# Optimization experiments

Hardware: AMD Instinct MI355X
Metric: run time of the kernel (lower is better)

Reference implementation:

```python
import jax, jax.numpy as jnp
import numpy as np

BLOCK_SIZE = 32
FP6_E2M3_MAX = 7.5

def _build_fp6_e2m3_grid():
    vals = set()
    for bits in range(64):
        s = (bits >> 5) & 1
        e = (bits >> 3) & 3
        m = bits & 7
        v = (m / 8.0) if e == 0 else (1.0 + m / 8.0) * 2.0 ** (e - 1)
        vals.add(-v if s else v)
    return np.array(sorted(vals), dtype=np.float32)

_GRID = jnp.asarray(_build_fp6_e2m3_grid())  # sorted 1-D fp32 grid (46 unique values)

def _nearest_on_grid(x, grid):
    # round-to-nearest on a sorted grid via searchsorted (matches torch reference)
    idx = jnp.clip(jnp.searchsorted(grid, x), 0, grid.shape[0] - 1)
    idx_lo = jnp.maximum(idx - 1, 0)
    v_hi = grid[idx]
    v_lo = grid[idx_lo]
    return jnp.where(jnp.abs(x - v_lo) <= jnp.abs(x - v_hi), v_lo, v_hi)

def _mx_quantize(t, eps=1e-30):
    # t: (rows, K) fp32, K divisible by BLOCK_SIZE
    rows, K = t.shape
    blocks = t.reshape(rows, K // BLOCK_SIZE, BLOCK_SIZE)
    scales = jnp.maximum(jnp.max(jnp.abs(blocks), axis=-1) / FP6_E2M3_MAX, eps)  # (rows, nb)
    q = _nearest_on_grid(blocks / scales[..., None], _GRID)  # fp6-simulated fp32
    return q, scales

def setup_inputs() -> dict:
    key = jax.random.key(0)
    k1, k2, k3 = jax.random.split(key, 3)
    x = jax.random.normal(k1, (8, 8192, 1024), dtype=jnp.float32)
    weight = jax.random.normal(k2, (1024, 1024), dtype=jnp.float32) * 0.02
    bias = jax.random.normal(k3, (1024,), dtype=jnp.float32) * 0.02
    return {"x": x, "weight": weight, "bias": bias}

def reference(x, weight, bias):
    batch_shape = x.shape[:-1]
    in_features = x.shape[-1]
    x2 = x.astype(jnp.float32).reshape(-1, in_features)      # (N, K)
    w2 = weight.astype(jnp.float32)                           # (J, K)
    xq, xs = _mx_quantize(x2)                                 # (N, nb, bs), (N, nb)
    wq, ws = _mx_quantize(w2)                                 # (J, nb, bs), (J, nb)
    # out[n, j] = sum_b xs[n,b] * ws[j,b] * dot(xq[n,b,:], wq[j,b,:])
    # == dequant(x) @ dequant(w).T  (fold fp32 scales into quantized blocks)
    xd = (xq * xs[..., None]).reshape(x2.shape)
    wd = (wq * ws[..., None]).reshape(w2.shape)
    out = xd @ wd.T + bias
    return out.reshape(*batch_shape, -1)
```

## Files before the change

kernel.cpp:

```cpp
#include <hip/hip_runtime.h>
#include <stdint.h>

#define K_DIM 1024
#define N_DIM 1024
#define M_DIM 65536

typedef __bf16 bf16_t;
typedef __bf16 bf16x8 __attribute__((ext_vector_type(8)));
typedef float f32x4 __attribute__((ext_vector_type(4)));

#define GLOAD_LDS16(g, l) __builtin_amdgcn_global_load_lds( \
    (const __attribute__((address_space(1))) void*)(g),     \
    (__attribute__((address_space(3))) void*)(l), 16, 0, 0)

__global__ __launch_bounds__(256) void quant_dequant_kernel(
    const float* __restrict__ in, bf16_t* __restrict__ out, long long nvec) {
  long long i = (long long)blockIdx.x * blockDim.x + threadIdx.x;
  long long stride = (long long)gridDim.x * blockDim.x;
  for (; i < nvec; i += stride) {
    long long base = i * 8;
    f32x4 v0 = *reinterpret_cast<const f32x4*>(in + base);
    f32x4 v1 = *reinterpret_cast<const f32x4*>(in + base + 4);
    float mx = 0.0f;
#pragma unroll
    for (int j = 0; j < 4; ++j) {
      mx = fmaxf(mx, fabsf(v0[j]));
      mx = fmaxf(mx, fabsf(v1[j]));
    }
    mx = fmaxf(mx, __shfl_xor(mx, 1));
    mx = fmaxf(mx, __shfl_xor(mx, 2));
    float s = fmaxf(mx / 7.5f, 1e-30f);
    bf16x8 o;
#pragma unroll
    for (int j = 0; j < 8; ++j) {
      float xv = (j < 4) ? v0[j] : v1[j - 4];
      float y = xv / s;
      float m = fabsf(y);
      float h, hinv;
      if (m < 2.0f)      { h = 0.125f; hinv = 8.0f; }
      else if (m < 4.0f) { h = 0.25f;  hinv = 4.0f; }
      else               { h = 0.5f;   hinv = 2.0f; }
      float n = m * hinv;
      float kf = floorf(n);
      float fr = n - kf;
      float up = (fr > 0.5f || (fr == 0.5f && y < 0.0f)) ? 1.0f : 0.0f;
      float q = fminf((kf + up) * h, 7.5f);
      o[j] = (bf16_t)(copysignf(q, y) * s);
    }
    *reinterpret_cast<bf16x8*>(out + base) = o;
  }
}

__global__ __launch_bounds__(256) void mx_gemm(
    const bf16_t* __restrict__ A, const bf16_t* __restrict__ B,
    const float* __restrict__ bias, float* __restrict__ C) {
  __shared__ bf16_t sA[128 * 32];
  __shared__ bf16_t sB[128 * 32];

  const int tid = threadIdx.x;
  const int lane = tid & 63;
  const int wid = tid >> 6;
  const int wm = wid >> 1;
  const int wn = wid & 1;

  const int b = blockIdx.x;
  const int xcd = b & 7;
  const int t = b >> 3;
  const int m_tile = xcd * 64 + (t >> 3);
  const int n_tile = t & 7;

  const bf16_t* Abase = A + (size_t)m_tile * 128 * K_DIM;
  const bf16_t* Bbase = B + (size_t)n_tile * 128 * K_DIM;

  f32x4 acc[4][4];
#pragma unroll
  for (int i = 0; i < 4; ++i)
#pragma unroll
    for (int j = 0; j < 4; ++j)
      acc[i][j] = (f32x4)(0.0f);

  int st_R[2], st_c8[2];
#pragma unroll
  for (int j = 0; j < 2; ++j) {
    int chunk = j * 4 + wid;
    int p = chunk * 1024 + lane * 16;
    int R = p >> 6;
    int T = (p >> 4) & 3;
    st_R[j] = R;
    st_c8[j] = (T ^ ((R >> 1) & 3)) << 3;
  }

  const int S = lane >> 4;
  int rdA[4], rdB[4];
#pragma unroll
  for (int i = 0; i < 4; ++i) {
    int Ra = wm * 64 + i * 16 + (lane & 15);
    rdA[i] = Ra * 64 + ((S ^ ((Ra >> 1) & 3)) << 4);
    int Rb = wn * 64 + i * 16 + (lane & 15);
    rdB[i] = Rb * 64 + ((S ^ ((Rb >> 1) & 3)) << 4);
  }

  for (int kt = 0; kt < K_DIM / 32; ++kt) {
    const int k0 = kt * 32;
#pragma unroll
    for (int j = 0; j < 2; ++j) {
      int chunk = j * 4 + wid;
      GLOAD_LDS16(Abase + (size_t)st_R[j] * K_DIM + k0 + st_c8[j],
                  sA + chunk * 512);
      GLOAD_LDS16(Bbase + (size_t)st_R[j] * K_DIM + k0 + st_c8[j],
                  sB + chunk * 512);
    }
    __syncthreads();

    bf16x8 af[4], bv[4];
#pragma unroll
    for (int i = 0; i < 4; ++i) {
      af[i] = *reinterpret_cast<const bf16x8*>(
          reinterpret_cast<const char*>(sA) + rdA[i]);
      bv[i] = *reinterpret_cast<const bf16x8*>(
          reinterpret_cast<const char*>(sB) + rdB[i]);
    }
#pragma unroll
    for (int i = 0; i < 4; ++i)
#pragma unroll
      for (int j = 0; j < 4; ++j)
        acc[i][j] =
            __builtin_amdgcn_mfma_f32_16x16x32_bf16(af[i], bv[j], acc[i][j],
                                                    0, 0, 0);
    __syncthreads();
  }

  const int col0 = n_tile * 128 + wn * 64 + (lane & 15);
  const int row0 = m_tile * 128 + wm * 64 + ((lane >> 4) << 2);
#pragma unroll
  for (int j = 0; j < 4; ++j) {
    float bvv = bias[col0 + j * 16];
#pragma unroll
    for (int i = 0; i < 4; ++i) {
#pragma unroll
      for (int r = 0; r < 4; ++r) {
        C[(size_t)(row0 + i * 16 + r) * N_DIM + col0 + j * 16] =
            acc[i][j][r] + bvv;
      }
    }
  }
}

extern "C" void kernel_launch(void* const* d_in, const int* in_sizes, int n_in,
                              void* d_out, int out_size, void* d_ws,
                              size_t ws_size, hipStream_t stream) {
  const float* x = (const float*)d_in[0];
  const float* w = (const float*)d_in[1];
  const float* bias = (const float*)d_in[2];
  float* out = (float*)d_out;

  bf16_t* xd = (bf16_t*)d_ws;
  bf16_t* wd = xd + (size_t)M_DIM * K_DIM;

  quant_dequant_kernel<<<4096, 256, 0, stream>>>(x, xd,
                                                 (long long)M_DIM * K_DIM / 8);
  quant_dequant_kernel<<<512, 256, 0, stream>>>(w, wd,
                                                (long long)K_DIM * N_DIM / 8);

  mx_gemm<<<(M_DIM / 128) * (N_DIM / 128), 256, 0, stream>>>(xd, wd, bias,
                                                             out);
}
```

Baseline: 316.9 us.

## Enlarge GEMM tiles to 256x256 with 4-stage async LDS pipeline

The bf16 GEMM now uses 512-thread blocks computing 256x256 output tiles, each wave holding a 128x64 accumulator. Global-to-LDS loads run through a four-deep ring buffer (128 KB LDS) with explicit vmcnt waits and a single barrier per k-step, instead of the old load/sync/compute/sync sequence. MFMA sections are wrapped in s_setprio. This aims to raise arithmetic intensity and hide global load latency, at the cost of higher register and LDS pressure, which allows only one block per CU given the LDS size.

```diff
diff --git a/kernel.cpp b/kernel.cpp
--- a/kernel.cpp
+++ b/kernel.cpp
@@ -12,6 +12,8 @@
 #define GLOAD_LDS16(g, l) __builtin_amdgcn_global_load_lds( \
     (const __attribute__((address_space(1))) void*)(g),     \
     (__attribute__((address_space(3))) void*)(l), 16, 0, 0)
+
+#define VMCNT(n) asm volatile("s_waitcnt vmcnt(%0)" ::"n"(n) : "memory")
 
 __global__ __launch_bounds__(256) void quant_dequant_kernel(
     const float* __restrict__ in, bf16_t* __restrict__ out, long long nvec) {
@@ -51,96 +53,116 @@
   }
 }
 
-__global__ __launch_bounds__(256) void mx_gemm(
+__global__ __launch_bounds__(512, 2) void mx_gemm(
     const bf16_t* __restrict__ A, const bf16_t* __restrict__ B,
     const float* __restrict__ bias, float* __restrict__ C) {
-  __shared__ bf16_t sA[128 * 32];
-  __shared__ bf16_t sB[128 * 32];
+  __shared__ char lds[131072];
 
   const int tid = threadIdx.x;
   const int lane = tid & 63;
   const int wid = tid >> 6;
-  const int wm = wid >> 1;
-  const int wn = wid & 1;
+  const int wm = wid >> 2;
+  const int wn = wid & 3;
 
   const int b = blockIdx.x;
   const int xcd = b & 7;
   const int t = b >> 3;
-  const int m_tile = xcd * 64 + (t >> 3);
-  const int n_tile = t & 7;
+  const int m_tile = xcd * 32 + (t >> 2);
+  const int n_tile = t & 3;
 
-  const bf16_t* Abase = A + (size_t)m_tile * 128 * K_DIM;
-  const bf16_t* Bbase = B + (size_t)n_tile * 128 * K_DIM;
+  const int R0 = tid >> 2;
+  const int c0 = ((tid & 3) ^ ((tid >> 2) & 3)) * 8;
+  const bf16_t* aS0 = A + (size_t)(m_tile * 256 + R0) * K_DIM + c0;
+  const bf16_t* aS1 = aS0 + (size_t)128 * K_DIM;
+  const bf16_t* bS0 = B + (size_t)(n_tile * 256 + R0) * K_DIM + c0;
+  const bf16_t* bS1 = bS0 + (size_t)128 * K_DIM;
+  const int dstOff = wid * 1024 + lane * 16;
 
-  f32x4 acc[4][4];
+  auto STAGE = [&](int u) {
+    char* sbase = lds + (u & 3) * 32768;
+    const int ko = u * 32;
+    GLOAD_LDS16(aS0 + ko, sbase + dstOff);
+    GLOAD_LDS16(aS1 + ko, sbase + 8192 + dstOff);
+    GLOAD_LDS16(bS0 + ko, sbase + 16384 + dstOff);
+    GLOAD_LDS16(bS1 + ko, sbase + 24576 + dstOff);
+  };
+
+  const int ps = (((lane >> 4) ^ (lane & 3)) << 4);
+  const int rowb = (lane & 15) * 64 + ps;
+  const int aOff = wm * 8192 + rowb;
+  const int bOff = 16384 + wn * 4096 + rowb;
+
+  f32x4 acc[8][4];
 #pragma unroll
-  for (int i = 0; i < 4; ++i)
+  for (int i = 0; i < 8; ++i)
+#pragma unroll
+    for (int j = 0; j < 4; ++j) acc[i][j] = (f32x4)(0.0f);
+
+  auto COMPUTE = [&](int u) {
+    const char* sbase = lds + (u & 3) * 32768;
+    bf16x8 bf[4], af[4];
 #pragma unroll
     for (int j = 0; j < 4; ++j)
-      acc[i][j] = (f32x4)(0.0f);
-
-  int st_R[2], st_c8[2];
+      bf[j] = *reinterpret_cast<const bf16x8*>(sbase + bOff + j * 1024);
 #pragma unroll
-  for (int j = 0; j < 2; ++j) {
-    int chunk = j * 4 + wid;
-    int p = chunk * 1024 + lane * 16;
-    int R = p >> 6;
-    int T = (p >> 4) & 3;
-    st_R[j] = R;
-    st_c8[j] = (T ^ ((R >> 1) & 3)) << 3;
-  }
-
-  const int S = lane >> 4;
-  int rdA[4], rdB[4];
-#pragma unroll
-  for (int i = 0; i < 4; ++i) {
-    int Ra = wm * 64 + i * 16 + (lane & 15);
-    rdA[i] = Ra * 64 + ((S ^ ((Ra >> 1) & 3)) << 4);
-    int Rb = wn * 64 + i * 16 + (lane & 15);
-    rdB[i] = Rb * 64 + ((S ^ ((Rb >> 1) & 3)) << 4);
-  }
-
-  for (int kt = 0; kt < K_DIM / 32; ++kt) {
-    const int k0 = kt * 32;
-#pragma unroll
-    for (int j = 0; j < 2; ++j) {
-      int chunk = j * 4 + wid;
-      GLOAD_LDS16(Abase + (size_t)st_R[j] * K_DIM + k0 + st_c8[j],
-                  sA + chunk * 512);
-      GLOAD_LDS16(Bbase + (size_t)st_R[j] * K_DIM + k0 + st_c8[j],
-                  sB + chunk * 512);
-    }
-    __syncthreads();
-
-    bf16x8 af[4], bv[4];
-#pragma unroll
-    for (int i = 0; i < 4; ++i) {
-      af[i] = *reinterpret_cast<const bf16x8*>(
-          reinterpret_cast<const char*>(sA) + rdA[i]);
-      bv[i] = *reinterpret_cast<const bf16x8*>(
-          reinterpret_cast<const char*>(sB) + rdB[i]);
-    }
+    for (int i = 0; i < 4; ++i)
+      af[i] = *reinterpret_cast<const bf16x8*>(sbase + aOff + i * 1024);
+    __builtin_amdgcn_s_setprio(1);
 #pragma unroll
     for (int i = 0; i < 4; ++i)
 #pragma unroll
       for (int j = 0; j < 4; ++j)
-        acc[i][j] =
-            __builtin_amdgcn_mfma_f32_16x16x32_bf16(af[i], bv[j], acc[i][j],
-                                                    0, 0, 0);
-    __syncthreads();
+        acc[i][j] = __builtin_amdgcn_mfma_f32_16x16x32_bf16(af[i], bf[j],
+                                                            acc[i][j], 0, 0, 0);
+    __builtin_amdgcn_s_setprio(0);
+#pragma unroll
+    for (int i = 0; i < 4; ++i)
+      af[i] = *reinterpret_cast<const bf16x8*>(sbase + aOff + 4096 + i * 1024);
+    __builtin_amdgcn_s_setprio(1);
+#pragma unroll
+    for (int i = 0; i < 4; ++i)
+#pragma unroll
+      for (int j = 0; j < 4; ++j)
+        acc[4 + i][j] = __builtin_amdgcn_mfma_f32_16x16x32_bf16(
+            af[i], bf[j], acc[4 + i][j], 0, 0, 0);
+    __builtin_amdgcn_s_setprio(0);
+  };
+
+  STAGE(0);
+  STAGE(1);
+  STAGE(2);
+
+  for (int kt = 0; kt < 29; ++kt) {
+    VMCNT(8);
+    __builtin_amdgcn_s_barrier();
+    __builtin_amdgcn_sched_barrier(0);
+    STAGE(kt + 3);
+    COMPUTE(kt);
   }
+  VMCNT(8);
+  __builtin_amdgcn_s_barrier();
+  __builtin_amdgcn_sched_barrier(0);
+  COMPUTE(29);
+  VMCNT(4);
+  __builtin_amdgcn_s_barrier();
+  __builtin_amdgcn_sched_barrier(0);
+  COMPUTE(30);
+  VMCNT(0);
+  __builtin_amdgcn_s_barrier();
+  __builtin_amdgcn_sched_barrier(0);
+  COMPUTE(31);
 
-  const int col0 = n_tile * 128 + wn * 64 + (lane & 15);
-  const int row0 = m_tile * 128 + wm * 64 + ((lane >> 4) << 2);
+  const int col0 = n_tile * 256 + wn * 64 + (lane & 15);
+  const int row0 = m_tile * 256 + wm * 128 + ((lane >> 4) << 2);
 #pragma unroll
   for (int j = 0; j < 4; ++j) {
-    float bvv = bias[col0 + j * 16];
+    float bv = bias[col0 + j * 16];
 #pragma unroll
-    for (int i = 0; i < 4; ++i) {
+    for (int m = 0; m < 8; ++m) {
 #pragma unroll
       for (int r = 0; r < 4; ++r) {
-        C[(size_t)(row0 + i * 16 + r) * N_DIM + col0 + j * 16] =
-            acc[i][j][r] + bvv;
+        C[(size_t)(row0 + m * 16 + r) * N_DIM + col0 + j * 16] =
+            acc[m][j][r] + bv;
       }
     }
   }
@@ -162,6 +184,6 @@
   quant_dequant_kernel<<<512, 256, 0, stream>>>(w, wd,
                                                 (long long)K_DIM * N_DIM / 8);
 
-  mx_gemm<<<(M_DIM / 128) * (N_DIM / 128), 256, 0, stream>>>(xd, wd, bias,
+  mx_gemm<<<(M_DIM / 256) * (N_DIM / 256), 512, 0, stream>>>(xd, wd, bias,
                                                              out);
 }
```

Measured after the change: 273.6 us. 13.7% less time.
